# Performance work log

Hardware: AMD Instinct MI355X
Metric: run time of the kernel (lower is better)

Reference implementation:

```python
import jax, jax.numpy as jnp
import numpy as np

H, L, N1, N2, N3 = 256, 141, 9, 34, 98
B, S = 64, 512

def setup_inputs() -> dict:
    key = jax.random.key(0)
    cnt = [0]
    def nrm(shape, s=0.05):
        cnt[0] += 1
        return jax.random.normal(jax.random.fold_in(key, cnt[0]), shape, jnp.float32) * s
    d = {}
    d['inputs'] = jax.random.randint(jax.random.fold_in(key, 1000), (B, S), 0, 30522)
    d['text_hidden'] = nrm((B, S, 768), 1.0)
    d['label_encoding'] = nrm((L, H), 1.0)
    d['w12'] = (jax.random.uniform(jax.random.fold_in(key, 1001), (N1, N2)) < 0.3).astype(jnp.float32)
    d['w23'] = (jax.random.uniform(jax.random.fold_in(key, 1002), (N2, N3)) < 0.3).astype(jnp.float32)
    d['fre12'] = jax.random.uniform(jax.random.fold_in(key, 1003), (N1, N2), jnp.float32)
    d['fre23'] = jax.random.uniform(jax.random.fold_in(key, 1004), (N2, N3), jnp.float32)
    for name in ['wi1', 'wf1', 'wo1', 'wu1', 'wi2', 'wf2', 'wo2', 'wu2']:
        d[name + '_W'] = nrm((H, H)); d[name + '_b'] = nrm((H,))
    for name in ['ui1', 'uf1', 'uo1', 'uu1', 'ui2', 'uf2', 'uo2', 'uu2']:
        d[name + '_W'] = nrm((H, H))
    d['mix_W'] = nrm((3 * H, H)); d['mix_b'] = nrm((H,))
    d['tt_W'] = nrm((768, H)); d['tt_b'] = nrm((H,))
    d['A'] = nrm((L, L)); d['Wp'] = nrm((H, H))
    d['out_W'] = nrm((L * H, L)); d['out_b'] = nrm((L,))
    return d

def reference(inputs, text_hidden, label_encoding, w12, w23, fre12, fre23,
              wi1_W, wi1_b, wf1_W, wf1_b, wo1_W, wo1_b, wu1_W, wu1_b,
              wi2_W, wi2_b, wf2_W, wf2_b, wo2_W, wo2_b, wu2_W, wu2_b,
              ui1_W, uf1_W, uo1_W, uu1_W, ui2_W, uf2_W, uo2_W, uu2_W,
              mix_W, mix_b, tt_W, tt_b, A, Wp, out_W, out_b):
    sig, tanh = jax.nn.sigmoid, jnp.tanh
    v1 = label_encoding[:N1]          # [N1,H]
    v2 = label_encoding[N1:N1 + N2]   # [N2,H]
    v3 = label_encoding[N1 + N2:]     # [N3,H]
    w21, w32 = w12.T, w23.T
    # --- top-down tree-LSTM (suffix 1) ---
    i11 = sig(v1 @ wi1_W + wi1_b); o11 = sig(v1 @ wo1_W + wo1_b); u11 = tanh(v1 @ wu1_W + wu1_b)
    c11 = i11 * u11; h11 = o11 * tanh(c11)
    h21t = w21 @ h11
    i21 = sig(v2 @ wi1_W + wi1_b + h21t @ ui1_W)
    f21 = sig(v2 @ wf1_W + wf1_b + h21t @ uf1_W)
    o21 = sig(v2 @ wo1_W + wo1_b + h21t @ uo1_W)
    u21 = tanh(v2 @ wu1_W + wu1_b + h21t @ uu1_W)
    c21 = i21 * u21 + f21 * (w21 @ c11); h21 = o21 * tanh(c21)
    h31t = w32 @ h21
    i31 = sig(v3 @ wi1_W + wi1_b + h31t @ ui1_W)
    f31 = sig(v3 @ wf1_W + wf1_b + h31t @ uf1_W)
    o31 = sig(v3 @ wo1_W + wo1_b + h31t @ uo1_W)
    u31 = tanh(v3 @ wu1_W + wu1_b + h31t @ uu1_W)
    c31 = i31 * u31 + f31 * (w32 @ c21); h31 = o31 * tanh(c31)
    # --- bottom-up tree-LSTM (suffix 2) ---
    i32 = sig(v3 @ wi2_W + wi2_b); o32 = sig(v3 @ wo2_W + wo2_b); u32 = tanh(v3 @ wu2_W + wu2_b)
    c32 = i32 * u32; h32 = o32 * tanh(c32)
    h22t = fre23 @ h32
    i22 = sig(v2 @ wi2_W + wi2_b + h22t @ ui2_W)
    f22 = sig((w32 @ v2) @ wf2_W + wf2_b + h32 @ uf2_W)   # [N3,H]
    o22 = sig(v2 @ wo2_W + wo2_b + h22t @ uo2_W)
    u22 = tanh(v2 @ wu2_W + wu2_b + h22t @ uu2_W)
    c22 = i22 * u22 + w23 @ (f22 * c32); h22 = o22 * tanh(c22)
    h12t = fre12 @ h22
    i12 = sig(v1 @ wi2_W + wi2_b + h12t @ ui2_W)
    f12 = sig((w21 @ v1) @ wf2_W + wf2_b + h22 @ uf2_W)   # [N2,H]
    o12 = sig(v1 @ wo2_W + wo2_b + h12t @ uo2_W)
    u12 = tanh(v1 @ wu2_W + wu2_b + h12t @ uu2_W)
    c12 = i12 * u12 + w12 @ (f12 * c22); h12 = o12 * tanh(c12)
    h1 = jnp.concatenate([h11, h12], axis=1)
    h2 = jnp.concatenate([h21, h22], axis=1)
    h3 = jnp.concatenate([h31, h32], axis=1)
    le = jnp.concatenate([h1, h2, h3], axis=0)            # [L,2H]
    temp = jax.nn.relu(A @ label_encoding @ Wp)           # [L,H]
    le = jnp.concatenate([le, temp], axis=1) @ mix_W + mix_b  # [L,H]
    # --- masked cross-attention pooling over text ---
    text = tanh(text_hidden @ tt_W + tt_b)                # [B,S,H]
    att = jnp.einsum('lh,bsh->bls', le, text)             # [B,L,S]
    pad = jnp.where((inputs == 0) | (inputs == 101) | (inputs == 102), -jnp.inf, 0.0).astype(text.dtype)
    att = jax.nn.softmax(att + pad[:, None, :], axis=2)
    features = jnp.einsum('bls,bsh->blh', att, text).reshape(inputs.shape[0], -1)  # [B,L*H]
    return sig(features @ out_W + out_b)                  # [B,L]
```

## Files before the change

### kernel.cpp

```cpp
#include <hip/hip_runtime.h>
#include <math.h>

static constexpr int H = 256, L = 141, N1 = 9, N2 = 34, N3 = 98;
static constexpr int B = 64, S = 512;

typedef __attribute__((ext_vector_type(8))) _Float16 f16x8;
typedef __attribute__((ext_vector_type(4))) float f32x4;

__device__ inline unsigned short f2h(float x) {
    _Float16 h = (_Float16)x;
    return __builtin_bit_cast(unsigned short, h);
}
__device__ inline float sigf(float x) { return 1.f / (1.f + __expf(-x)); }

__device__ inline void gload_lds16(const void* g, void* l) {
    __builtin_amdgcn_global_load_lds(
        (const __attribute__((address_space(1))) void*)g,
        (__attribute__((address_space(3))) void*)l, 16, 0, 0);
}

__global__ __launch_bounds__(256) void conv_ttW(
    const float* __restrict__ W, unsigned short* __restrict__ Bt)
{
    __shared__ unsigned short Tl[32][257];
    const int t = blockIdx.x, tid = threadIdx.x;
    #pragma unroll
    for (int p = 0; p < 32; p++) {
        int lin = p * 256 + tid;
        int r = lin >> 8, c = lin & 255;
        Tl[r][c] = f2h(W[(long)(t * 32 + r) * 256 + c]);
    }
    __syncthreads();
    unsigned short v[32];
    #pragma unroll
    for (int kin = 0; kin < 32; kin++) v[kin] = Tl[kin][tid];
    uint4* dst = (uint4*)(Bt + ((long)t * 256 + tid) * 32);
    #pragma unroll
    for (int q = 0; q < 4; q++) dst[q] = ((const uint4*)v)[q];
}

__global__ __launch_bounds__(512, 4) void text_gemm3(
    const float* __restrict__ Af,
    const unsigned short* __restrict__ Bt,
    const float* __restrict__ bias,
    unsigned short* __restrict__ outH,
    unsigned short* __restrict__ outHT)
{
    __shared__ unsigned short smem[28672];
    unsigned short* As = smem;
    unsigned short* Bs = smem + 4096;
    unsigned short* T  = smem;

    const int tid  = threadIdx.x;
    const int wave = tid >> 6, lane = tid & 63;
    const int quad = lane >> 4, l16 = lane & 15;
    const int m0 = blockIdx.x * 64;
    const int wm = (wave >> 2) * 32;
    const int wn = (wave & 3) * 64;

    const int arow = tid >> 3;
    const int ac16 = tid & 7;
    const float* aSrc = Af + (long)(m0 + arow) * 768 + ac16 * 4;
    const int ac8d = ac16 ^ ((arow & 3) << 1);
    const int aWoff = arow * 32 + ac8d * 4;

    const int bsc = (lane & 3) ^ ((lane >> 3) & 3);
    const long bSrcOff0 = (long)(wave * 32 + (lane >> 2)) * 32 + bsc * 8;
    const long bSrcOff1 = bSrcOff0 + 16 * 32;
    const int bDst0 = (wave * 32) * 32, bDst1 = (wave * 32 + 16) * 32;

    int aro[2], bro[4];
    #pragma unroll
    for (int i = 0; i < 2; i++) {
        int r = wm + i * 16 + l16;
        aro[i] = r * 32 + ((quad * 2) ^ ((r & 3) << 1)) * 4;
    }
    #pragma unroll
    for (int j = 0; j < 4; j++) {
        int n = wn + j * 16 + l16;
        bro[j] = n * 32 + ((quad ^ ((n >> 1) & 3)) << 3);
    }

    f32x4 acc[2][4] = {};
    float4 ar0, ar1;

    auto issueB = [&](int kt, int pb) {
        const unsigned short* src = Bt + (long)kt * 8192;
        unsigned short* d = Bs + pb * 8192;
        gload_lds16(src + bSrcOff0, d + bDst0);
        gload_lds16(src + bSrcOff1, d + bDst1);
    };
    auto writeA = [&](const float4& v, int pa) {
        unsigned int p0 = f2h(v.x) | ((unsigned int)f2h(v.y) << 16);
        unsigned int p1 = f2h(v.z) | ((unsigned int)f2h(v.w) << 16);
        *(uint2*)&As[pa * 2048 + aWoff] = make_uint2(p0, p1);
    };

    ar0 = *(const float4*)(aSrc + 0 * 32);
    issueB(0, 0);
    ar1 = *(const float4*)(aSrc + 1 * 32);
    issueB(1, 1);
    asm volatile("s_waitcnt vmcnt(5)" ::: "memory");
    writeA(ar0, 0);
    asm volatile("s_waitcnt vmcnt(3)" ::: "memory");
    asm volatile("s_waitcnt lgkmcnt(0)" ::: "memory");
    asm volatile("s_barrier" ::: "memory");

    auto body = [&](int t, float4& arIn, float4& arOut, int pa, int pr) {
        int kt2 = (t + 2 <= 23) ? t + 2 : 23;
        arOut = *(const float4*)(aSrc + kt2 * 32);
        f16x8 a[2], b[4];
        const unsigned short* ab = As + pa * 2048;
        const unsigned short* bb = Bs + pr * 8192;
        #pragma unroll
        for (int i = 0; i < 2; i++) a[i] = *(const f16x8*)&ab[aro[i]];
        #pragma unroll
        for (int j = 0; j < 4; j++) b[j] = *(const f16x8*)&bb[bro[j]];
        #pragma unroll
        for (int i = 0; i < 2; i++)
            #pragma unroll
            for (int j = 0; j < 4; j++)
                acc[i][j] = __builtin_amdgcn_mfma_f32_16x16x32_f16(
                    a[i], b[j], acc[i][j], 0, 0, 0);
        asm volatile("s_waitcnt vmcnt(3)" ::: "memory");
        writeA(arIn, pa ^ 1);
        int pw = pr + 2; if (pw >= 3) pw -= 3;
        issueB(kt2, pw);
        asm volatile("s_waitcnt vmcnt(3)" ::: "memory");
        asm volatile("s_waitcnt lgkmcnt(0)" ::: "memory");
        asm volatile("s_barrier" ::: "memory");
    };

    int pr = 0;
    #pragma unroll 1
    for (int t = 0; t < 24; t += 2) {
        body(t,     ar1, ar0, t & 1 ? 1 : 0, pr);
        int pr1 = pr + 1; if (pr1 >= 3) pr1 -= 3;
        body(t + 1, ar0, ar1, 1, pr1);
        pr = pr1 + 1; if (pr >= 3) pr -= 3;
    }
    asm volatile("s_waitcnt vmcnt(0)" ::: "memory");
    __syncthreads();

    float bv[4];
    #pragma unroll
    for (int j = 0; j < 4; j++) bv[j] = bias[wn + j * 16 + l16];

    #pragma unroll
    for (int i = 0; i < 2; i++) {
        #pragma unroll
        for (int j = 0; j < 4; j++) {
            const int mlb = wm + i * 16 + quad * 4;
            const int n   = wn + j * 16 + l16;
            unsigned short hv[4];
            #pragma unroll
            for (int r = 0; r < 4; r++) {
                float v = tanhf(acc[i][j][r] + bv[j]);
                hv[r] = f2h(v);
                outH[(long)(m0 + mlb + r) * 256 + n] = hv[r];
            }
            uint2 p;
            p.x = hv[0] | ((unsigned int)hv[1] << 16);
            p.y = hv[2] | ((unsigned int)hv[3] << 16);
            *(uint2*)&T[n * 72 + mlb] = p;
        }
    }
    __syncthreads();
    {
        const int bb2 = m0 >> 9, s0 = m0 & 511;
        const int n = tid >> 1, half = tid & 1;
        const uint4* src = (const uint4*)&T[n * 72 + half * 32];
        uint4* dst = (uint4*)&outHT[((long)bb2 * 256 + n) * 512 + s0 + half * 32];
        dst[0] = src[0]; dst[1] = src[1];
        dst[2] = src[2]; dst[3] = src[3];
    }
}

template<int EPI, bool CONVA, int IM>
__global__ __launch_bounds__(256) void gemm_mfma(
    const void* __restrict__ Aptr, int lda, long strA,
    const unsigned short* __restrict__ Bp, int ldb, long strB,
    float* __restrict__ C, int ldc, long strC,
    int M, int N, int K,
    const float* __restrict__ bias,
    const int* __restrict__ tokens,
    unsigned short* __restrict__ outH,
    unsigned short* __restrict__ outHT,
    int kChunk)
{
    __shared__ unsigned short A_s[32 * IM * 32];
    __shared__ unsigned short B_s[128 * 32];
    __shared__ unsigned short T[EPI == 1 ? 128 * 64 : 1];
    const int tid  = threadIdx.x;
    const int wave = tid >> 6, lane = tid & 63;
    const int quad = lane >> 4, l16 = lane & 15;
    const int bz = blockIdx.z;
    const int m0 = blockIdx.y * (32 * IM), n0 = blockIdx.x * 128;
    const int wm = (wave & 1) * (16 * IM), wn = (wave >> 1) * 64;

    long aBase, bBase;
    int kBeg, kEnd;
    if (EPI == 4) { aBase = 0; bBase = 0; kBeg = bz * kChunk; kEnd = kBeg + kChunk; }
    else { aBase = (long)bz * strA; bBase = (long)bz * strB; kBeg = 0; kEnd = K; }

    f32x4 acc[IM][4] = {};

    for (int k0 = kBeg; k0 < kEnd; k0 += 32) {
        if (CONVA) {
            const float* Af = (const float*)Aptr + aBase;
            #pragma unroll
            for (int it = 0; it < IM; it++) {
                int idx = it * 256 + tid;
                int row = idx >> 3, col4 = idx & 7;
                int gm = m0 + row; if (gm > M - 1) gm = M - 1;
                float4 v = *(const float4*)(Af + (long)gm * lda + k0 + col4 * 4);
                unsigned int p0 = f2h(v.x) | ((unsigned int)f2h(v.y) << 16);
                unsigned int p1 = f2h(v.z) | ((unsigned int)f2h(v.w) << 16);
                *(uint2*)&A_s[row * 32 + col4 * 4] = make_uint2(p0, p1);
            }
        } else {
            const unsigned short* Ab = (const unsigned short*)Aptr + aBase;
            #pragma unroll
            for (int t = 0; t < IM / 2; t++) {
                int rowb = wave * (8 * IM) + t * 16;
                int gm = m0 + rowb + (lane >> 2); if (gm > M - 1) gm = M - 1;
                gload_lds16(Ab + (long)gm * lda + k0 + (lane & 3) * 8,
                            &A_s[rowb * 32]);
            }
        }
        #pragma unroll
        for (int t = 0; t < 2; t++) {
            int rowb = wave * 32 + t * 16;
            int gn = n0 + rowb + (lane >> 2); if (gn > N - 1) gn = N - 1;
            gload_lds16(Bp + bBase + (long)gn * ldb + k0 + (lane & 3) * 8,
                        &B_s[rowb * 32]);
        }
        __syncthreads();
        f16x8 a[IM], b[4];
        #pragma unroll
        for (int i = 0; i < IM; i++)
            a[i] = *(const f16x8*)&A_s[(wm + i * 16 + l16) * 32 + quad * 8];
        #pragma unroll
        for (int j = 0; j < 4; j++)
            b[j] = *(const f16x8*)&B_s[(wn + j * 16 + l16) * 32 + quad * 8];
        #pragma unroll
        for (int i = 0; i < IM; i++)
            #pragma unroll
            for (int j = 0; j < 4; j++)
                acc[i][j] = __builtin_amdgcn_mfma_f32_16x16x32_f16(
                    a[i], b[j], acc[i][j], 0, 0, 0);
        __syncthreads();
    }

    #pragma unroll
    for (int i = 0; i < IM; i++) {
        #pragma unroll
        for (int j = 0; j < 4; j++) {
            #pragma unroll
            for (int r = 0; r < 4; r++) {
                int ml = wm + i * 16 + quad * 4 + r;
                int nl = wn + j * 16 + l16;
                int gm = m0 + ml, gn = n0 + nl;
                if (gm >= M || gn >= N) continue;
                float v = acc[i][j][r];
                if (EPI == 1) {
                    v = tanhf(v + bias[gn]);
                    unsigned short hv = f2h(v);
                    outH[(long)gm * ldc + gn] = hv;
                    T[nl * 64 + ml] = hv;
                } else if (EPI == 2) {
                    int tok = tokens[(long)bz * 512 + gn];
                    if (tok == 0 || tok == 101 || tok == 102) v -= 1e30f;
                    C[(long)bz * strC + (long)gm * ldc + gn] = v;
                } else if (EPI == 3) {
                    outH[(long)bz * strC + (long)gm * ldc + gn] = f2h(v);
                } else {
                    C[(long)bz * strC + (long)gm * ldc + gn] = v;
                }
            }
        }
    }
    if (EPI == 1) {
        __syncthreads();
        int bb = m0 >> 9, s0 = m0 & 511;
        int rr = tid >> 1, half = tid & 1;
        const uint4* srcp = (const uint4*)&T[rr * 64 + half * 32];
        uint4* dstp = (uint4*)&outHT[((long)bb * 256 + n0 + rr) * 512 + s0 + half * 32];
        dstp[0] = srcp[0]; dstp[1] = srcp[1]; dstp[2] = srcp[2]; dstp[3] = srcp[3];
    }
}

__global__ __launch_bounds__(256) void transp_t64(
    const float* __restrict__ src, unsigned short* __restrict__ dst,
    int R, int C)
{
    __shared__ unsigned short T[64 * 65];
    const int tid = threadIdx.x;
    const int r0 = blockIdx.x * 64, c0 = blockIdx.y * 64;
    #pragma unroll
    for (int p = 0; p < 16; p++) {
        int lin = p * 256 + tid;
        int r = lin >> 6, c = lin & 63;
        int gc = c0 + c;
        float v = (gc < C) ? src[(long)(r0 + r) * C + gc] : 0.f;
        T[c * 65 + r] = f2h(v);
    }
    __syncthreads();
    #pragma unroll
    for (int p = 0; p < 16; p++) {
        int lin = p * 256 + tid;
        int c = lin >> 6, r = lin & 63;
        if (c0 + c < C)
            dst[(long)(c0 + c) * R + r0 + r] = T[c * 65 + r];
    }
}

__global__ __launch_bounds__(256) void gate_pre(
    const float* __restrict__ le,
    const float* W0, const float* W1, const float* W2, const float* W3,
    const float* W4, const float* W5, const float* W6,
    const float* b0, const float* b1, const float* b2, const float* b3,
    const float* b4, const float* b5, const float* b6,
    float* __restrict__ G)
{
    __shared__ float ls[256];
    __shared__ float red[256];
    const int j = blockIdx.x >> 2, x = blockIdx.x & 3, m = blockIdx.y;
    const int tid = threadIdx.x, nl = tid & 63, ks = tid >> 6, n = x * 64 + nl;
    ls[tid] = le[(long)m * 256 + tid];
    __syncthreads();
    const float *W, *bb;
    switch (j) {
        case 0: W = W0; bb = b0; break;  case 1: W = W1; bb = b1; break;
        case 2: W = W2; bb = b2; break;  case 3: W = W3; bb = b3; break;
        case 4: W = W4; bb = b4; break;  case 5: W = W5; bb = b5; break;
        default: W = W6; bb = b6;
    }
    float a0 = 0, a1 = 0, a2 = 0, a3 = 0;
    for (int k = ks; k + 12 < 256; k += 16) {
        long o = (long)k * 256 + n;
        a0 += ls[k] * W[o];        a1 += ls[k + 4] * W[o + 1024];
        a2 += ls[k + 8] * W[o + 2048]; a3 += ls[k + 12] * W[o + 3072];
    }
    red[tid] = a0 + a1 + a2 + a3;
    __syncthreads();
    if (ks == 0)
        G[((long)j * 141 + m) * 256 + n] =
            red[nl] + red[64 + nl] + red[128 + nl] + red[192 + nl] + bb[n];
}

__global__ __launch_bounds__(256) void pre2(
    const float* __restrict__ A, const float* __restrict__ le,
    const float* __restrict__ w23, const float* __restrict__ w12,
    const float* __restrict__ Wp, const float* __restrict__ wf2_W,
    float* __restrict__ tmpP, float* __restrict__ wv2f, float* __restrict__ wv1f)
{
    __shared__ float cs[141];
    __shared__ float t[256];
    __shared__ float red[256];
    const int x = blockIdx.x, y = blockIdx.y;
    const int tid = threadIdx.x, nl = tid & 63, ks = tid >> 6, n = x * 64 + nl;
    int job, m, K1;
    if (y < 141)      { job = 0; m = y;       K1 = 141; }
    else if (y < 239) { job = 1; m = y - 141; K1 = 34; }
    else              { job = 2; m = y - 239; K1 = 9; }
    if (tid < K1)
        cs[tid] = (job == 0) ? A[(long)m * 141 + tid]
                : (job == 1) ? w23[(long)tid * 98 + m]
                             : w12[(long)tid * 34 + m];
    __syncthreads();
    const float* s1 = (job == 1) ? le + 9 * 256 : le;
    float acc = 0;
    #pragma unroll 4
    for (int k = 0; k < K1; k++) acc += cs[k] * s1[(long)k * 256 + tid];
    t[tid] = acc;
    __syncthreads();
    const float* W = (job == 0) ? Wp : wf2_W;
    float a0 = 0, a1 = 0, a2 = 0, a3 = 0;
    for (int k = ks; k + 12 < 256; k += 16) {
        long o = (long)k * 256 + n;
        a0 += t[k] * W[o];        a1 += t[k + 4] * W[o + 1024];
        a2 += t[k + 8] * W[o + 2048]; a3 += t[k + 12] * W[o + 3072];
    }
    red[tid] = a0 + a1 + a2 + a3;
    __syncthreads();
    if (ks == 0) {
        float tot = red[nl] + red[64 + nl] + red[128 + nl] + red[192 + nl];
        if (job == 0)      tmpP[(long)m * 256 + n] = fmaxf(tot, 0.f);
        else if (job == 1) wv2f[(long)m * 256 + n] = tot;
        else               wv1f[(long)m * 256 + n] = tot;
    }
}

__global__ __launch_bounds__(256) void ew1(
    const float* __restrict__ G, float* __restrict__ h11, float* __restrict__ c11,
    float* __restrict__ h32, float* __restrict__ c32)
{
    int y = blockIdx.x, n = threadIdx.x;
    if (y < 9) {
        int m = y;
        float iv = sigf(G[(0L * 141 + m) * 256 + n]);
        float ov = sigf(G[(2L * 141 + m) * 256 + n]);
        float uv = tanhf(G[(3L * 141 + m) * 256 + n]);
        float cv = iv * uv;
        c11[m * 256 + n] = cv; h11[m * 256 + n] = ov * tanhf(cv);
    } else {
        int r = y - 9, grow = 43 + r;
        float iv = sigf(G[(4L * 141 + grow) * 256 + n]);
        float ov = sigf(G[(5L * 141 + grow) * 256 + n]);
        float uv = tanhf(G[(6L * 141 + grow) * 256 + n]);
        float cv = iv * uv;
        c32[r * 256 + n] = cv; h32[r * 256 + n] = ov * tanhf(cv);
    }
}

__global__ __launch_bounds__(256) void chain_mm(int phase,
    const float* __restrict__ w12, const float* __restrict__ w23,
    const float* __restrict__ fre23, const float* __restrict__ fre12,
    const float* __restrict__ h11, const float* __restrict__ c11,
    const float* __restrict__ h32,
    const float* __restrict__ h21, const float* __restrict__ c21,
    const float* __restrict__ h22,
    const float* __restrict__ wv2f, const float* __restrict__ wv1f,
    const float* __restrict__ wf2_b, const float* __restrict__ uf2_W,
    const float* __restrict__ c32, const float* __restrict__ c22,
    float* __restrict__ h21t, float* __restrict__ c21p,
    float* __restrict__ h22t, float* __restrict__ fcb,
    float* __restrict__ h31t, float* __restrict__ c31p,
    float* __restrict__ h12t, float* __restrict__ fc2b)
{
    __shared__ float cs[256];
    __shared__ float red[256];
    const int x = blockIdx.x, y = blockIdx.y;
    const int tid = threadIdx.x, nl = tid & 63, ks = tid >> 6, n = x * 64 + nl;
    int job, m;
    if (phase == 0) {
        if (y < 34)       { job = 0; m = y; }
        else if (y < 68)  { job = 1; m = y - 34; }
        else if (y < 102) { job = 2; m = y - 68; }
        else              { job = 3; m = y - 102; }
    } else {
        if (y < 98)       { job = 0; m = y; }
        else if (y < 196) { job = 1; m = y - 98; }
        else if (y < 205) { job = 2; m = y - 196; }
        else              { job = 3; m = y - 205; }
    }
    if (job < 3) {
        int K; const float* src; float* dst;
        if (phase == 0) {
            K = (job == 2) ? 98 : 9;
            src = (job == 0) ? h11 : (job == 1) ? c11 : h32;
            dst = (job == 0) ? h21t : (job == 1) ? c21p : h22t;
            if (tid < K)
                cs[tid] = (job == 2) ? fre23[(long)m * 98 + tid]
                                     : w12[(long)tid * 34 + m];
        } else {
            K = 34;
            src = (job == 0) ? h21 : (job == 1) ? c21 : h22;
            dst = (job == 0) ? h31t : (job == 1) ? c31p : h12t;
            if (tid < K)
                cs[tid] = (job == 2) ? fre12[(long)m * 34 + tid]
                                     : w23[(long)tid * 98 + m];
        }
        __syncthreads();
        float a0 = 0;
        for (int k = ks; k < K; k += 4) a0 += cs[k] * src[(long)k * 256 + n];
        red[tid] = a0;
        __syncthreads();
        if (ks == 0)
            dst[(long)m * 256 + n] = red[nl] + red[64 + nl] + red[128 + nl] + red[192 + nl];
    } else {
        const float* row = (phase == 0) ? h32 + m * 256 : h22 + m * 256;
        const float* pre = (phase == 0) ? wv2f : wv1f;
        const float* cm  = (phase == 0) ? c32 : c22;
        float* dst       = (phase == 0) ? fcb : fc2b;
        cs[tid] = row[tid];
        __syncthreads();
        float a0 = 0, a1 = 0, a2 = 0, a3 = 0;
        for (int k = ks; k + 12 < 256; k += 16) {
            long o = (long)k * 256 + n;
            a0 += cs[k] * uf2_W[o];        a1 += cs[k + 4] * uf2_W[o + 1024];
            a2 += cs[k + 8] * uf2_W[o + 2048]; a3 += cs[k + 12] * uf2_W[o + 3072];
        }
        red[tid] = a0 + a1 + a2 + a3;
        __syncthreads();
        if (ks == 0) {
            float tot = red[nl] + red[64 + nl] + red[128 + nl] + red[192 + nl]
                      + pre[(long)m * 256 + n] + wf2_b[n];
            dst[(long)m * 256 + n] = sigf(tot) * cm[(long)m * 256 + n];
        }
    }
}

__global__ __launch_bounds__(256) void lstm_fused(int phase,
    const float* __restrict__ G,
    const float* __restrict__ h21t, const float* __restrict__ c21p,
    const float* __restrict__ h22t, const float* __restrict__ fcb,
    const float* __restrict__ h31t, const float* __restrict__ c31p,
    const float* __restrict__ h12t, const float* __restrict__ fc2b,
    const float* __restrict__ w23, const float* __restrict__ w12,
    const float* __restrict__ ui1, const float* __restrict__ uf1,
    const float* __restrict__ uo1, const float* __restrict__ uu1,
    const float* __restrict__ ui2, const float* __restrict__ uo2,
    const float* __restrict__ uu2,
    float* __restrict__ h21, float* __restrict__ c21,
    float* __restrict__ h22, float* __restrict__ c22,
    float* __restrict__ h31, float* __restrict__ h12)
{
    __shared__ float hs[256];
    __shared__ float cs[128];
    __shared__ float red[1024];
    const int x = blockIdx.x, y = blockIdx.y;
    const int tid = threadIdx.x, nl = tid & 63, ks = tid >> 6, n = x * 64 + nl;
    bool modef; int m, grow, Kx = 0;
    const float *hrow, *U0, *U1, *U2, *U3 = nullptr, *Sx = nullptr, *cmod = nullptr;
    float *ho, *co = nullptr;
    if (phase == 0) {
        if (y < 34) { modef = true;  m = y;      grow = 9 + m;  hrow = h21t;
                      U0 = ui1; U1 = uf1; U2 = uo1; U3 = uu1; cmod = c21p; ho = h21; co = c21; }
        else        { modef = false; m = y - 34; grow = 9 + m;  hrow = h22t;
                      U0 = ui2; U1 = uo2; U2 = uu2; Sx = fcb; Kx = 98; ho = h22; co = c22;
                      if (tid < 98) cs[tid] = w23[(long)m * 98 + tid]; }
    } else {
        if (y < 98) { modef = true;  m = y;      grow = 43 + m; hrow = h31t;
                      U0 = ui1; U1 = uf1; U2 = uo1; U3 = uu1; cmod = c31p; ho = h31; co = nullptr; }
        else        { modef = false; m = y - 98; grow = m;      hrow = h12t;
                      U0 = ui2; U1 = uo2; U2 = uu2; Sx = fc2b; Kx = 34; ho = h12; co = nullptr;
                      if (tid < 34) cs[tid] = w12[(long)m * 34 + tid]; }
    }
    hs[tid] = hrow[(long)m * 256 + tid];
    __syncthreads();
    float a0 = 0, a1 = 0, a2 = 0, a3 = 0;
    if (modef) {
        for (int k = ks; k < 256; k += 4) {
            float xv = hs[k]; long o = (long)k * 256 + n;
            a0 += xv * U0[o]; a1 += xv * U1[o]; a2 += xv * U2[o]; a3 += xv * U3[o];
        }
    } else {
        for (int k = ks; k < 256; k += 4) {
            float xv = hs[k]; long o = (long)k * 256 + n;
            a0 += xv * U0[o]; a1 += xv * U1[o]; a2 += xv * U2[o];
        }
        for (int k = ks; k < Kx; k += 4) a3 += cs[k] * Sx[(long)k * 256 + n];
    }
    red[tid] = a0; red[256 + tid] = a1; red[512 + tid] = a2; red[768 + tid] = a3;
    __syncthreads();
    if (ks == 0) {
        float t0 = 0, t1 = 0, t2 = 0, t3 = 0;
        #pragma unroll
        for (int s2 = 0; s2 < 4; s2++) {
            t0 += red[s2 * 64 + nl];       t1 += red[256 + s2 * 64 + nl];
            t2 += red[512 + s2 * 64 + nl]; t3 += red[768 + s2 * 64 + nl];
        }
        if (modef) {
            float ti = t0 + G[(0L * 141 + grow) * 256 + n];
            float tf = t1 + G[(1L * 141 + grow) * 256 + n];
            float to = t2 + G[(2L * 141 + grow) * 256 + n];
            float tu = t3 + G[(3L * 141 + grow) * 256 + n];
            float cv = sigf(ti) * tanhf(tu) + sigf(tf) * cmod[(long)m * 256 + n];
            ho[(long)m * 256 + n] = sigf(to) * tanhf(cv);
            if (co) co[(long)m * 256 + n] = cv;
        } else {
            float ti = t0 + G[(4L * 141 + grow) * 256 + n];
            float to = t1 + G[(5L * 141 + grow) * 256 + n];
            float tu = t2 + G[(6L * 141 + grow) * 256 + n];
            float cv = sigf(ti) * tanhf(tu) + t3;
            ho[(long)m * 256 + n] = sigf(to) * tanhf(cv);
            if (co) co[(long)m * 256 + n] = cv;
        }
    }
}

__global__ __launch_bounds__(256) void mix_mm(
    const float* __restrict__ h11, const float* __restrict__ h12,
    const float* __restrict__ h21, const float* __restrict__ h22,
    const float* __restrict__ h31, const float* __restrict__ h32,
    const float* __restrict__ tmpP, const float* __restrict__ mix_W,
    const float* __restrict__ mix_b, unsigned short* __restrict__ le_h)
{
    __shared__ float ls[768];
    __shared__ float red[256];
    const int x = blockIdx.x, l = blockIdx.y;
    const int tid = threadIdx.x, nl = tid & 63, ks = tid >> 6, n = x * 64 + nl;
    const float *pa, *pb; int r;
    if (l < 9)       { pa = h11; pb = h12; r = l; }
    else if (l < 43) { pa = h21; pb = h22; r = l - 9; }
    else             { pa = h31; pb = h32; r = l - 43; }
    for (int j = tid; j < 768; j += 256) {
        float v;
        if (j < 256)      v = pa[r * 256 + j];
        else if (j < 512) v = pb[r * 256 + (j - 256)];
        else              v = tmpP[l * 256 + (j - 512)];
        ls[j] = v;
    }
    __syncthreads();
    float a0 = 0, a1 = 0, a2 = 0, a3 = 0;
    for (int k = ks; k + 12 < 768; k += 16) {
        long o = (long)k * 256 + n;
        a0 += ls[k] * mix_W[o];        a1 += ls[k + 4] * mix_W[o + 1024];
        a2 += ls[k + 8] * mix_W[o + 2048]; a3 += ls[k + 12] * mix_W[o + 3072];
    }
    red[tid] = a0 + a1 + a2 + a3;
    __syncthreads();
    if (ks == 0) {
        float tot = red[nl] + red[64 + nl] + red[128 + nl] + red[192 + nl] + mix_b[n];
        le_h[(long)l * 256 + n] = f2h(tot);
    }
}

__global__ __launch_bounds__(256) void softmax512(
    const float* __restrict__ att, unsigned short* __restrict__ atth)
{
    __shared__ float red[256];
    const float* row = att + (long)blockIdx.x * 512;
    unsigned short* orow = atth + (long)blockIdx.x * 512;
    int t = threadIdx.x;
    float a = row[t], b = row[t + 256];
    red[t] = fmaxf(a, b);
    __syncthreads();
    for (int s = 128; s > 0; s >>= 1) {
        if (t < s) red[t] = fmaxf(red[t], red[t + s]);
        __syncthreads();
    }
    float m = red[0];
    __syncthreads();
    float ea = __expf(a - m), eb = __expf(b - m);
    red[t] = ea + eb;
    __syncthreads();
    for (int s = 128; s > 0; s >>= 1) {
        if (t < s) red[t] += red[t + s];
        __syncthreads();
    }
    float inv = 1.f / red[0];
    orow[t] = f2h(ea * inv);
    orow[t + 256] = f2h(eb * inv);
}

__global__ __launch_bounds__(256) void out_final(
    const float* __restrict__ acc, const float* __restrict__ ob,
    float* __restrict__ out, int total, int nz)
{
    int i = blockIdx.x * 256 + threadIdx.x;
    if (i >= total) return;
    float v = ob[i % L];
    #pragma unroll 4
    for (int z = 0; z < nz; z++) v += acc[(long)z * total + i];
    out[i] = sigf(v);
}

extern "C" void kernel_launch(void* const* d_in, const int* in_sizes, int n_in,
                              void* d_out, int out_size, void* d_ws, size_t ws_size,
                              hipStream_t stream)
{
    (void)in_sizes; (void)n_in; (void)out_size; (void)ws_size;
    const int*   inputs      = (const int*)d_in[0];
    const float* text_hidden = (const float*)d_in[1];
    const float* label_enc   = (const float*)d_in[2];
    const float* w12   = (const float*)d_in[3];
    const float* w23   = (const float*)d_in[4];
    const float* fre12 = (const float*)d_in[5];
    const float* fre23 = (const float*)d_in[6];
    const float* wi1_W = (const float*)d_in[7],  *wi1_b = (const float*)d_in[8];
    const float* wf1_W = (const float*)d_in[9],  *wf1_b = (const float*)d_in[10];
    const float* wo1_W = (const float*)d_in[11], *wo1_b = (const float*)d_in[12];
    const float* wu1_W = (const float*)d_in[13], *wu1_b = (const float*)d_in[14];
    const float* wi2_W = (const float*)d_in[15], *wi2_b = (const float*)d_in[16];
    const float* wf2_W = (const float*)d_in[17], *wf2_b = (const float*)d_in[18];
    const float* wo2_W = (const float*)d_in[19], *wo2_b = (const float*)d_in[20];
    const float* wu2_W = (const float*)d_in[21], *wu2_b = (const float*)d_in[22];
    const float* ui1_W = (const float*)d_in[23], *uf1_W = (const float*)d_in[24];
    const float* uo1_W = (const float*)d_in[25], *uu1_W = (const float*)d_in[26];
    const float* ui2_W = (const float*)d_in[27], *uf2_W = (const float*)d_in[28];
    const float* uo2_W = (const float*)d_in[29], *uu2_W = (const float*)d_in[30];
    const float* mix_W = (const float*)d_in[31], *mix_b = (const float*)d_in[32];
    const float* tt_W  = (const float*)d_in[33], *tt_b  = (const float*)d_in[34];
    const float* Amat  = (const float*)d_in[35], *Wp    = (const float*)d_in[36];
    const float* out_W = (const float*)d_in[37], *out_b = (const float*)d_in[38];
    float* out = (float*)d_out;

    float* ws = (float*)d_ws;
    float* att     = ws; ws += (long)B * L * S;
    unsigned short* text_h  = (unsigned short*)ws; ws += (long)B * S * H / 2;
    unsigned short* text_hT = (unsigned short*)ws; ws += (long)B * S * H / 2;
    unsigned short* att_h   = (unsigned short*)ws; ws += (long)B * L * S / 2;
    unsigned short* tt_Wt   = (unsigned short*)ws; ws += 768 * H / 2;
    unsigned short* le_h    = (unsigned short*)ws; ws += L * H / 2 + 4;
    unsigned short* out_Wh  = (unsigned short*)ws; ws += (long)L * 36096 / 2;
    unsigned short* feat_h  = (unsigned short*)ws; ws += (long)B * L * H / 2;
    float* outacc = ws; ws += (long)B * L * 141;
    float* G    = ws; ws += 7 * 141 * 256;
    float* tmpP = ws; ws += L * H;
    float* wv2f = ws; ws += N3 * H;
    float* wv1f = ws; ws += N2 * H;
    float* h11  = ws; ws += N1 * H;  float* c11  = ws; ws += N1 * H;
    float* h21  = ws; ws += N2 * H;  float* c21  = ws; ws += N2 * H;
    float* h21t = ws; ws += N2 * H;  float* c21p = ws; ws += N2 * H;
    float* h31  = ws; ws += N3 * H;  float* h31t = ws; ws += N3 * H;
    float* c31p = ws; ws += N3 * H;
    float* h32  = ws; ws += N3 * H;  float* c32  = ws; ws += N3 * H;
    float* h22  = ws; ws += N2 * H;  float* c22  = ws; ws += N2 * H;
    float* h22t = ws; ws += N2 * H;  float* fcb  = ws; ws += N3 * H;
    float* h12  = ws; ws += N1 * H;  float* h12t = ws; ws += N1 * H;
    float* fc2b = ws; ws += N2 * H;

    conv_ttW<<<24, 256, 0, stream>>>(tt_W, tt_Wt);
    text_gemm3<<<512, 512, 0, stream>>>(
        text_hidden, tt_Wt, tt_b, text_h, text_hT);
    gate_pre<<<dim3(28, 141), 256, 0, stream>>>(label_enc,
        wi1_W, wf1_W, wo1_W, wu1_W, wi2_W, wo2_W, wu2_W,
        wi1_b, wf1_b, wo1_b, wu1_b, wi2_b, wo2_b, wu2_b, G);
    pre2<<<dim3(4, 273), 256, 0, stream>>>(Amat, label_enc, w23, w12, Wp, wf2_W,
        tmpP, wv2f, wv1f);
    transp_t64<<<dim3(36096 / 64, 3), 256, 0, stream>>>(out_W, out_Wh, 36096, 141);
    ew1<<<107, 256, 0, stream>>>(G, h11, c11, h32, c32);
    chain_mm<<<dim3(4, 200), 256, 0, stream>>>(0, w12, w23, fre23, fre12,
        h11, c11, h32, h21, c21, h22, wv2f, wv1f, wf2_b, uf2_W, c32, c22,
        h21t, c21p, h22t, fcb, h31t, c31p, h12t, fc2b);
    lstm_fused<<<dim3(4, 68), 256, 0, stream>>>(0, G,
        h21t, c21p, h22t, fcb, h31t, c31p, h12t, fc2b, w23, w12,
        ui1_W, uf1_W, uo1_W, uu1_W, ui2_W, uo2_W, uu2_W,
        h21, c21, h22, c22, h31, h12);
    chain_mm<<<dim3(4, 239), 256, 0, stream>>>(1, w12, w23, fre23, fre12,
        h11, c11, h32, h21, c21, h22, wv2f, wv1f, wf2_b, uf2_W, c32, c22,
        h21t, c21p, h22t, fcb, h31t, c31p, h12t, fc2b);
    lstm_fused<<<dim3(4, 107), 256, 0, stream>>>(1, G,
        h21t, c21p, h22t, fcb, h31t, c31p, h12t, fc2b, w23, w12,
        ui1_W, uf1_W, uo1_W, uu1_W, ui2_W, uo2_W, uu2_W,
        h21, c21, h22, c22, h31, h12);
    mix_mm<<<dim3(4, 141), 256, 0, stream>>>(h11, h12, h21, h22, h31, h32,
        tmpP, mix_W, mix_b, le_h);
    gemm_mfma<2, false, 2><<<dim3(S / 128, (L + 63) / 64, B), 256, 0, stream>>>(
        le_h, H, 0, text_h, H, (long)S * H, att, S, (long)L * S,
        L, S, H, nullptr, inputs, nullptr, nullptr, 0);
    softmax512<<<B * L, 256, 0, stream>>>(att, att_h);
    gemm_mfma<3, false, 2><<<dim3(H / 128, (L + 63) / 64, B), 256, 0, stream>>>(
        att_h, S, (long)L * S, text_hT, S, (long)H * S, nullptr, H, (long)L * H,
        L, H, S, nullptr, nullptr, feat_h, nullptr, 0);
    gemm_mfma<4, false, 2><<<dim3(2, 1, 141), 256, 0, stream>>>(
        feat_h, L * H, 0, out_Wh, L * H, 0, outacc, L, (long)B * L,
        B, L, L * H, nullptr, nullptr, nullptr, nullptr, 256);
    out_final<<<(B * L + 255) / 256, 256, 0, stream>>>(outacc, out_b, out, B * L, 141);
}
```

Before: 462.6 us.

## Fuse attention score GEMM, masked softmax and value GEMM into one kernel

```diff
diff --git a/kernel.cpp b/kernel.cpp
--- a/kernel.cpp
+++ b/kernel.cpp
@@ -174,6 +174,142 @@
         dst[0] = src[0]; dst[1] = src[1];
         dst[2] = src[2]; dst[3] = src[3];
     }
+}
+
+__global__ __launch_bounds__(512, 4) void fused_att(
+    const unsigned short* __restrict__ le_h,
+    const unsigned short* __restrict__ text_h,
+    const unsigned short* __restrict__ text_hT,
+    const int* __restrict__ tokens,
+    unsigned short* __restrict__ feat_h)
+{
+    __shared__ unsigned short P[16 * 520];
+    __shared__ float maskv[512];
+    __shared__ float redm[8][16];
+    __shared__ float reds[8][16];
+    const int tid  = threadIdx.x;
+    const int wave = tid >> 6, lane = tid & 63;
+    const int quad = lane >> 4, l16 = lane & 15;
+    const int m0 = blockIdx.x * 16;
+    const int b  = blockIdx.y;
+
+    {
+        int tok = tokens[(long)b * 512 + tid];
+        maskv[tid] = (tok == 0 || tok == 101 || tok == 102) ? -1e30f : 0.f;
+    }
+
+    int arow = m0 + l16; if (arow > L - 1) arow = L - 1;
+    const unsigned short* ap = le_h + (long)arow * 256 + quad * 8;
+    f16x8 a[8];
+    #pragma unroll
+    for (int ks = 0; ks < 8; ks++)
+        a[ks] = *(const f16x8*)(ap + ks * 32);
+
+    const unsigned short* bp =
+        text_h + ((long)b * 512 + wave * 64 + l16) * 256 + quad * 8;
+    f32x4 acc[4] = {};
+    #pragma unroll 2
+    for (int ks = 0; ks < 8; ks++) {
+        f16x8 bf[4];
+        #pragma unroll
+        for (int j = 0; j < 4; j++)
+            bf[j] = *(const f16x8*)(bp + (long)j * 16 * 256 + ks * 32);
+        #pragma unroll
+        for (int j = 0; j < 4; j++)
+            acc[j] = __builtin_amdgcn_mfma_f32_16x16x32_f16(
+                a[ks], bf[j], acc[j], 0, 0, 0);
+    }
+    __syncthreads();
+
+    float mv[4];
+    #pragma unroll
+    for (int j = 0; j < 4; j++) mv[j] = maskv[wave * 64 + j * 16 + l16];
+    #pragma unroll
+    for (int j = 0; j < 4; j++)
+        #pragma unroll
+        for (int r = 0; r < 4; r++) acc[j][r] += mv[j];
+
+    float vmax[4];
+    #pragma unroll
+    for (int r = 0; r < 4; r++)
+        vmax[r] = fmaxf(fmaxf(acc[0][r], acc[1][r]),
+                        fmaxf(acc[2][r], acc[3][r]));
+    #pragma unroll
+    for (int d = 1; d <= 8; d <<= 1)
+        #pragma unroll
+        for (int r = 0; r < 4; r++)
+            vmax[r] = fmaxf(vmax[r], __shfl_xor(vmax[r], d));
+    if (l16 == 0) {
+        #pragma unroll
+        for (int r = 0; r < 4; r++) redm[wave][quad * 4 + r] = vmax[r];
+    }
+    __syncthreads();
+    float M[4];
+    #pragma unroll
+    for (int r = 0; r < 4; r++) {
+        float v = redm[0][quad * 4 + r];
+        #pragma unroll
+        for (int w = 1; w < 8; w++) v = fmaxf(v, redm[w][quad * 4 + r]);
+        M[r] = v;
+    }
+
+    float vsum[4] = {0.f, 0.f, 0.f, 0.f};
+    #pragma unroll
+    for (int j = 0; j < 4; j++)
+        #pragma unroll
+        for (int r = 0; r < 4; r++) {
+            float e = __expf(acc[j][r] - M[r]);
+            acc[j][r] = e;
+            vsum[r] += e;
+        }
+    #pragma unroll
+    for (int d = 1; d <= 8; d <<= 1)
+        #pragma unroll
+        for (int r = 0; r < 4; r++) vsum[r] += __shfl_xor(vsum[r], d);
+    if (l16 == 0) {
+        #pragma unroll
+        for (int r = 0; r < 4; r++) reds[wave][quad * 4 + r] = vsum[r];
+    }
+    __syncthreads();
+    #pragma unroll
+    for (int r = 0; r < 4; r++) {
+        float s = 0.f;
+        #pragma unroll
+        for (int w = 0; w < 8; w++) s += reds[w][quad * 4 + r];
+        M[r] = 1.f / s;
+    }
+
+    #pragma unroll
+    for (int j = 0; j < 4; j++)
+        #pragma unroll
+        for (int r = 0; r < 4; r++)
+            P[(quad * 4 + r) * 520 + wave * 64 + j * 16 + l16] =
+                f2h(acc[j][r] * M[r]);
+    __syncthreads();
+
+    const unsigned short* vp =
+        text_hT + ((long)b * 256 + wave * 32 + l16) * 512 + quad * 8;
+    f32x4 accp[2] = {};
+    #pragma unroll 4
+    for (int ks = 0; ks < 16; ks++) {
+        f16x8 pa = *(const f16x8*)&P[l16 * 520 + ks * 32 + quad * 8];
+        f16x8 v0 = *(const f16x8*)(vp + ks * 32);
+        f16x8 v1 = *(const f16x8*)(vp + 16 * 512 + ks * 32);
+        accp[0] = __builtin_amdgcn_mfma_f32_16x16x32_f16(pa, v0, accp[0], 0, 0, 0);
+        accp[1] = __builtin_amdgcn_mfma_f32_16x16x32_f16(pa, v1, accp[1], 0, 0, 0);
+    }
+
+    #pragma unroll
+    for (int j2 = 0; j2 < 2; j2++)
+        #pragma unroll
+        for (int r = 0; r < 4; r++) {
+            int row = m0 + quad * 4 + r;
+            if (row < L) {
+                int h = wave * 32 + j2 * 16 + l16;
+                feat_h[(long)b * (L * H) + (long)row * 256 + h] =
+                    f2h(accp[j2][r]);
+            }
+        }
 }
 
 template<int EPI, bool CONVA, int IM>
@@ -263,12 +399,7 @@
                 int gm = m0 + ml, gn = n0 + nl;
                 if (gm >= M || gn >= N) continue;
                 float v = acc[i][j][r];
-                if (EPI == 1) {
-                    v = tanhf(v + bias[gn]);
-                    unsigned short hv = f2h(v);
-                    outH[(long)gm * ldc + gn] = hv;
-                    T[nl * 64 + ml] = hv;
-                } else if (EPI == 2) {
+                if (EPI == 2) {
                     int tok = tokens[(long)bz * 512 + gn];
                     if (tok == 0 || tok == 101 || tok == 102) v -= 1e30f;
                     C[(long)bz * strC + (long)gm * ldc + gn] = v;
@@ -279,14 +410,6 @@
                 }
             }
         }
-    }
-    if (EPI == 1) {
-        __syncthreads();
-        int bb = m0 >> 9, s0 = m0 & 511;
-        int rr = tid >> 1, half = tid & 1;
-        const uint4* srcp = (const uint4*)&T[rr * 64 + half * 32];
-        uint4* dstp = (uint4*)&outHT[((long)bb * 256 + n0 + rr) * 512 + s0 + half * 32];
-        dstp[0] = srcp[0]; dstp[1] = srcp[1]; dstp[2] = srcp[2]; dstp[3] = srcp[3];
     }
 }
 
@@ -606,34 +729,6 @@
         float tot = red[nl] + red[64 + nl] + red[128 + nl] + red[192 + nl] + mix_b[n];
         le_h[(long)l * 256 + n] = f2h(tot);
     }
-}
-
-__global__ __launch_bounds__(256) void softmax512(
-    const float* __restrict__ att, unsigned short* __restrict__ atth)
-{
-    __shared__ float red[256];
-    const float* row = att + (long)blockIdx.x * 512;
-    unsigned short* orow = atth + (long)blockIdx.x * 512;
-    int t = threadIdx.x;
-    float a = row[t], b = row[t + 256];
-    red[t] = fmaxf(a, b);
-    __syncthreads();
-    for (int s = 128; s > 0; s >>= 1) {
-        if (t < s) red[t] = fmaxf(red[t], red[t + s]);
-        __syncthreads();
-    }
-    float m = red[0];
-    __syncthreads();
-    float ea = __expf(a - m), eb = __expf(b - m);
-    red[t] = ea + eb;
-    __syncthreads();
-    for (int s = 128; s > 0; s >>= 1) {
-        if (t < s) red[t] += red[t + s];
-        __syncthreads();
-    }
-    float inv = 1.f / red[0];
-    orow[t] = f2h(ea * inv);
-    orow[t + 256] = f2h(eb * inv);
 }
 
 __global__ __launch_bounds__(256) void out_final(
@@ -702,6 +797,7 @@
     float* h22t = ws; ws += N2 * H;  float* fcb  = ws; ws += N3 * H;
     float* h12  = ws; ws += N1 * H;  float* h12t = ws; ws += N1 * H;
     float* fc2b = ws; ws += N2 * H;
+    (void)att; (void)att_h;
 
     conv_ttW<<<24, 256, 0, stream>>>(tt_W, tt_Wt);
     text_gemm3<<<512, 512, 0, stream>>>(
@@ -729,13 +825,8 @@
         h21, c21, h22, c22, h31, h12);
     mix_mm<<<dim3(4, 141), 256, 0, stream>>>(h11, h12, h21, h22, h31, h32,
         tmpP, mix_W, mix_b, le_h);
-    gemm_mfma<2, false, 2><<<dim3(S / 128, (L + 63) / 64, B), 256, 0, stream>>>(
-        le_h, H, 0, text_h, H, (long)S * H, att, S, (long)L * S,
-        L, S, H, nullptr, inputs, nullptr, nullptr, 0);
-    softmax512<<<B * L, 256, 0, stream>>>(att, att_h);
-    gemm_mfma<3, false, 2><<<dim3(H / 128, (L + 63) / 64, B), 256, 0, stream>>>(
-        att_h, S, (long)L * S, text_hT, S, (long)H * S, nullptr, H, (long)L * H,
-        L, H, S, nullptr, nullptr, feat_h, nullptr, 0);
+    fused_att<<<dim3(9, 64), 512, 0, stream>>>(
+        le_h, text_h, text_hT, inputs, feat_h);
     gemm_mfma<4, false, 2><<<dim3(2, 1, 141), 256, 0, stream>>>(
         feat_h, L * H, 0, out_Wh, L * H, 0, outacc, L, (long)B * L,
         B, L, L * H, nullptr, nullptr, nullptr, nullptr, 256);
```

Result: slower. 606.4 us (+31.1%).

## Add dedicated attention-logits MFMA kernel with resident A tile and triple-buffered B

Applied to the files above, without the earlier changes.

```diff
diff --git a/kernel.cpp b/kernel.cpp
--- a/kernel.cpp
+++ b/kernel.cpp
@@ -176,6 +176,106 @@
     }
 }
 
+__global__ __launch_bounds__(512, 4) void att_logits(
+    const unsigned short* __restrict__ le_h,
+    const unsigned short* __restrict__ text_h,
+    const int* __restrict__ tokens,
+    float* __restrict__ att)
+{
+    __shared__ unsigned short A_s[64 * 256];
+    __shared__ unsigned short Bs[3][256 * 32];
+    const int tid  = threadIdx.x;
+    const int wave = tid >> 6, lane = tid & 63;
+    const int quad = lane >> 4, l16 = lane & 15;
+    const int s0 = blockIdx.x * 256;
+    const int m0 = blockIdx.y * 64;
+    const int b  = blockIdx.z;
+    const int wm = (wave >> 2) * 32;
+    const int wn = (wave & 3) * 64;
+
+    const int bsc = (lane & 3) ^ ((lane >> 3) & 3);
+    const long bOff0 = (long)(b * 512 + s0 + wave * 32 + (lane >> 2)) * 256 + bsc * 8;
+    const long bOff1 = bOff0 + 16 * 256;
+    const int bDst0 = (wave * 32) * 32, bDst1 = bDst0 + 16 * 32;
+    auto issueB = [&](int kt, int pb) {
+        gload_lds16(text_h + bOff0 + kt * 32, &Bs[pb][bDst0]);
+        gload_lds16(text_h + bOff1 + kt * 32, &Bs[pb][bDst1]);
+    };
+
+    int abase[2], axm[2], bro[4];
+    #pragma unroll
+    for (int i = 0; i < 2; i++) {
+        int r = wm + i * 16 + l16;
+        abase[i] = r * 256; axm[i] = r & 7;
+    }
+    #pragma unroll
+    for (int j = 0; j < 4; j++) {
+        int n = wn + j * 16 + l16;
+        bro[j] = n * 32 + ((quad ^ ((n >> 1) & 3)) << 3);
+    }
+
+    #pragma unroll
+    for (int p = 0; p < 4; p++) {
+        int row = p * 16 + (tid >> 5);
+        int c   = tid & 31;
+        int grow = m0 + row; if (grow > L - 1) grow = L - 1;
+        gload_lds16(le_h + (long)grow * 256 + ((c ^ (row & 7)) << 3),
+                    A_s + p * 4096 + wave * 512);
+    }
+    issueB(0, 0);
+    issueB(1, 1);
+    asm volatile("s_waitcnt vmcnt(2)" ::: "memory");
+    asm volatile("s_barrier" ::: "memory");
+
+    f32x4 acc[2][4] = {};
+    #pragma unroll 1
+    for (int t = 0; t < 8; t++) {
+        const int pr = t % 3;
+        f16x8 a[2], b[4];
+        #pragma unroll
+        for (int i = 0; i < 2; i++)
+            a[i] = *(const f16x8*)&A_s[abase[i] + (((t * 4 + quad) ^ axm[i]) << 3)];
+        const unsigned short* bb = &Bs[pr][0];
+        #pragma unroll
+        for (int j = 0; j < 4; j++) b[j] = *(const f16x8*)&bb[bro[j]];
+        #pragma unroll
+        for (int i = 0; i < 2; i++)
+            #pragma unroll
+            for (int j = 0; j < 4; j++)
+                acc[i][j] = __builtin_amdgcn_mfma_f32_16x16x32_f16(
+                    a[i], b[j], acc[i][j], 0, 0, 0);
+        if (t < 7) {
+            int kt2 = (t + 2 <= 7) ? t + 2 : 7;
+            int pw = (t + 2) % 3;
+            issueB(kt2, pw);
+            asm volatile("s_waitcnt vmcnt(2)" ::: "memory");
+            asm volatile("s_barrier" ::: "memory");
+        }
+    }
+    asm volatile("s_waitcnt vmcnt(0)" ::: "memory");
+
+    float mvv[4];
+    #pragma unroll
+    for (int j = 0; j < 4; j++) {
+        int gs = s0 + wn + j * 16 + l16;
+        int tok = tokens[(long)b * 512 + gs];
+        mvv[j] = (tok == 0 || tok == 101 || tok == 102) ? 1e30f : 0.f;
+    }
+    #pragma unroll
+    for (int i = 0; i < 2; i++)
+        #pragma unroll
+        for (int j = 0; j < 4; j++)
+            #pragma unroll
+            for (int r = 0; r < 4; r++) {
+                int gm = m0 + wm + i * 16 + quad * 4 + r;
+                if (gm < L) {
+                    int gs = s0 + wn + j * 16 + l16;
+                    att[(long)b * (L * S) + (long)gm * 512 + gs] =
+                        acc[i][j][r] - mvv[j];
+                }
+            }
+}
+
 template<int EPI, bool CONVA, int IM>
 __global__ __launch_bounds__(256) void gemm_mfma(
     const void* __restrict__ Aptr, int lda, long strA,
@@ -190,7 +290,6 @@
 {
     __shared__ unsigned short A_s[32 * IM * 32];
     __shared__ unsigned short B_s[128 * 32];
-    __shared__ unsigned short T[EPI == 1 ? 128 * 64 : 1];
     const int tid  = threadIdx.x;
     const int wave = tid >> 6, lane = tid & 63;
     const int quad = lane >> 4, l16 = lane & 15;
@@ -263,12 +362,7 @@
                 int gm = m0 + ml, gn = n0 + nl;
                 if (gm >= M || gn >= N) continue;
                 float v = acc[i][j][r];
-                if (EPI == 1) {
-                    v = tanhf(v + bias[gn]);
-                    unsigned short hv = f2h(v);
-                    outH[(long)gm * ldc + gn] = hv;
-                    T[nl * 64 + ml] = hv;
-                } else if (EPI == 2) {
+                if (EPI == 2) {
                     int tok = tokens[(long)bz * 512 + gn];
                     if (tok == 0 || tok == 101 || tok == 102) v -= 1e30f;
                     C[(long)bz * strC + (long)gm * ldc + gn] = v;
@@ -279,14 +373,6 @@
                 }
             }
         }
-    }
-    if (EPI == 1) {
-        __syncthreads();
-        int bb = m0 >> 9, s0 = m0 & 511;
-        int rr = tid >> 1, half = tid & 1;
-        const uint4* srcp = (const uint4*)&T[rr * 64 + half * 32];
-        uint4* dstp = (uint4*)&outHT[((long)bb * 256 + n0 + rr) * 512 + s0 + half * 32];
-        dstp[0] = srcp[0]; dstp[1] = srcp[1]; dstp[2] = srcp[2]; dstp[3] = srcp[3];
     }
 }
 
@@ -729,9 +815,8 @@
         h21, c21, h22, c22, h31, h12);
     mix_mm<<<dim3(4, 141), 256, 0, stream>>>(h11, h12, h21, h22, h31, h32,
         tmpP, mix_W, mix_b, le_h);
-    gemm_mfma<2, false, 2><<<dim3(S / 128, (L + 63) / 64, B), 256, 0, stream>>>(
-        le_h, H, 0, text_h, H, (long)S * H, att, S, (long)L * S,
-        L, S, H, nullptr, inputs, nullptr, nullptr, 0);
+    att_logits<<<dim3(2, 3, 64), 512, 0, stream>>>(
+        le_h, text_h, inputs, att);
     softmax512<<<B * L, 256, 0, stream>>>(att, att_h);
     gemm_mfma<3, false, 2><<<dim3(H / 128, (L + 63) / 64, B), 256, 0, stream>>>(
         att_h, S, (long)L * S, text_hT, S, (long)H * S, nullptr, H, (long)L * H,
```

After: 453.3 us. 1.02x faster.
